# Performance work log

Hardware: AMD Instinct MI355X
Metric: run time of the kernel (lower is better)

## Reference

```python
import jax, jax.numpy as jnp
import numpy as np

B, C, L, H, W_SP = 4, 768, 8, 14, 14
HEADS = 12
HD = C // HEADS  # 64
SCALE = HD ** (-0.5)


def setup_inputs() -> dict:
    key = jax.random.key(0)
    ks = jax.random.split(key, 8)
    return {
        "q": jax.random.normal(ks[0], (B, C, L, H, W_SP), dtype=jnp.float32),
        "k": jax.random.normal(ks[1], (B, C, L, H, W_SP), dtype=jnp.float32),
        "v": jax.random.normal(ks[2], (B, C, L, H, W_SP), dtype=jnp.float32),
        "cls_q": jax.random.normal(ks[3], (B, C), dtype=jnp.float32),
        "cls_k": jax.random.normal(ks[4], (B, C), dtype=jnp.float32),
        "cls_v": jax.random.normal(ks[5], (B, C), dtype=jnp.float32),
        "W": jax.random.normal(ks[6], (C, C), dtype=jnp.float32) * 0.02,
        "b": jnp.zeros((C,), dtype=jnp.float32),
    }


def _split_heads(t):
    # 'b (head c) l h w -> b head (l h w) c'
    Bx = t.shape[0]
    return t.reshape(Bx, HEADS, HD, -1).transpose(0, 1, 3, 2)


def _split_cls(t):
    # 'b (head c) -> b head 1 c'
    return t.reshape(t.shape[0], HEADS, 1, HD)


def reference(q, k, v, cls_q, cls_k, cls_v, W, b):
    out_l, out_h, out_w = q.shape[2], q.shape[3], q.shape[4]
    qh = jnp.concatenate([_split_cls(cls_q), _split_heads(q)], axis=2)  # [B,head,S,c]
    kh = jnp.concatenate([_split_cls(cls_k), _split_heads(k)], axis=2)
    vh = jnp.concatenate([_split_cls(cls_v), _split_heads(v)], axis=2)
    attn = jnp.einsum('bhqc,bhkc->bhqk', qh, kh) * SCALE  # [B,head,S,S]
    attn = jax.nn.softmax(attn, axis=-1)
    x = jnp.einsum('bhqk,bhkc->bhqc', attn, vh)           # [B,head,S,c]
    Bx, _, S, _ = x.shape
    x = x.transpose(0, 2, 1, 3).reshape(Bx, S, HEADS * HD)  # 'b h s c -> b s (h c)'
    x = x @ W.T + b  # nn.Linear
    class_token = x[:, 0, :]
    x = x[:, 1:, :]
    # 'b (l h w) c -> b c l h w'
    x = x.transpose(0, 2, 1).reshape(Bx, HEADS * HD, out_l, out_h, out_w)
    return (x, class_token)
```

## Files before the change

### kernel.cpp

```cpp
#include <hip/hip_runtime.h>
#include <hip/hip_bf16.h>

#define NSP   1568
#define SEQ   1569
#define CDIM  768
#define NHEAD 12
#define NTOT  6276
#define BATCH 4
#define NBH   48
#define SPADQ 1664
#define SPADK 1664

typedef __bf16 bf16x8 __attribute__((ext_vector_type(8)));
typedef float  f32x4  __attribute__((ext_vector_type(4)));

static __device__ __forceinline__ unsigned pkbf(float a, float b) {
    __hip_bfloat16 ha = __float2bfloat16(a), hb = __float2bfloat16(b);
    return (unsigned)*(unsigned short*)&ha | ((unsigned)*(unsigned short*)&hb << 16);
}

__global__ __launch_bounds__(256) void pack_all(
    const float* __restrict__ qg, const float* __restrict__ kg,
    const float* __restrict__ vg, const float* __restrict__ cq,
    const float* __restrict__ ck, const float* __restrict__ cv,
    const float* __restrict__ W,
    __hip_bfloat16* __restrict__ Qb, __hip_bfloat16* __restrict__ Kb,
    __hip_bfloat16* __restrict__ Vb, __hip_bfloat16* __restrict__ Wb)
{
    const int t  = threadIdx.x;
    const int z  = blockIdx.z;

    if (z == 3) {
        const int id = blockIdx.y * 26 + blockIdx.x;
        if (id >= 288) return;
        const size_t i = ((size_t)id * 256 + t) * 8;
        const float4 a = *(const float4*)(W + i);
        const float4 c = *(const float4*)(W + i + 4);
        __hip_bfloat16 hh[8] = {
            __float2bfloat16(a.x), __float2bfloat16(a.y),
            __float2bfloat16(a.z), __float2bfloat16(a.w),
            __float2bfloat16(c.x), __float2bfloat16(c.y),
            __float2bfloat16(c.z), __float2bfloat16(c.w)};
        *(uint4*)(Wb + i) = *(const uint4*)hh;
        return;
    }

    const int st = blockIdx.x;
    const int bh = blockIdx.y;
    const int b = bh / NHEAD, h = bh % NHEAD;

    if (z == 2) {
        const float* g = vg + ((size_t)b * CDIM + h * 64) * NSP;
        const float* c = cv + b * CDIM + h * 64;
        const int sl = t & 63, s = st * 64 + sl;
        for (int i = 0; i < 16; ++i) {
            const int d = (t >> 6) * 16 + i;
            float v = 0.f;
            if (s == 0)       v = c[d];
            else if (s < SEQ) v = g[(size_t)d * NSP + s - 1];
            Vb[((size_t)bh * 64 + d) * SPADK + s] = __float2bfloat16(v);
        }
        return;
    }

    __shared__ float tile[64 * 65];
    const float* g = (z ? kg : qg) + ((size_t)b * CDIM + h * 64) * NSP;
    const float* c = (z ? ck : cq) + b * CDIM + h * 64;
    const float scale = z ? 1.f : 0.125f * 1.44269504f;

    const int sl = t & 63, s = st * 64 + sl;
    for (int i = 0; i < 16; ++i) {
        const int d = (t >> 6) * 16 + i;
        float v = 0.f;
        if (s == 0)       v = c[d];
        else if (s < SEQ) v = g[(size_t)d * NSP + s - 1];
        tile[d * 65 + sl] = v * scale;
    }
    __syncthreads();
    __hip_bfloat16* out = z ? Kb : Qb;
    const size_t rowbase = (size_t)bh * (z ? SPADK : SPADQ) + st * 64;
    const int d = t & 63;
    for (int i = 0; i < 16; ++i) {
        const int r = i * 4 + (t >> 6);
        out[(rowbase + r) * 64 + d] = __float2bfloat16(tile[d * 65 + r]);
    }
}

__global__ __launch_bounds__(256, 3) void attn_mfma(
    const __hip_bfloat16* __restrict__ Qbp, const __hip_bfloat16* __restrict__ Kbp,
    const __hip_bfloat16* __restrict__ Vbp, __hip_bfloat16* __restrict__ xb)
{
    __shared__ char smem[49152];
    char* const Ksb0 = smem;
    char* const Ksb1 = smem + 16384;

    const int t    = threadIdx.x;
    const int lane = t & 63;
    const int w    = t >> 6;
    const int lo   = lane & 15, hi = lane >> 4;

    const int gid  = blockIdx.x;
    const int slot = gid >> 3;
    const int bh   = (gid & 7) + 8 * (slot / 13);
    const int qb   = (slot % 13) * 128;
    const int b    = bh / NHEAD, h = bh % NHEAD;

    const unsigned short* Qg = (const unsigned short*)Qbp + ((size_t)bh * SPADQ + qb) * 64;
    const unsigned short* Kg = (const unsigned short*)Kbp + (size_t)bh * SPADK * 64;
    const unsigned short* Vg = (const unsigned short*)Vbp + (size_t)bh * 64 * SPADK;

    char* const Pw = smem + 32768 + w * 4096;

    bf16x8 qf[2][2];
    #pragma unroll
    for (int qn = 0; qn < 2; ++qn)
        #pragma unroll
        for (int ks = 0; ks < 2; ++ks)
            qf[qn][ks] = *(const bf16x8*)(Qg + (w * 32 + qn * 16 + lo) * 64 + (ks * 4 + hi) * 8);

    f32x4 o[2][4];
    f32x4 l5[2];
    #pragma unroll
    for (int m = 0; m < 2; ++m) {
        l5[m] = (f32x4){0.f, 0.f, 0.f, 0.f};
        #pragma unroll
        for (int n = 0; n < 4; ++n) o[m][n] = (f32x4){0.f, 0.f, 0.f, 0.f};
    }

    bf16x8 ones;
    #pragma unroll
    for (int i = 0; i < 8; ++i) ones[i] = (__bf16)1.0f;

    const int sr = t >> 3, sc = t & 7;

    uint4 kreg[4];
    #pragma unroll
    for (int p = 0; p < 4; ++p)
        kreg[p] = *(const uint4*)(Kg + (size_t)(sr + 32 * p) * 64 + sc * 8);
    #pragma unroll
    for (int p = 0; p < 4; ++p) {
        const int r = sr + 32 * p;
        *(uint4*)(Ksb0 + r * 128 + ((sc ^ (r & 7)) * 16)) = kreg[p];
    }

    int cur = 0;

    for (int it = 0; it < 13; ++it) {
        __syncthreads();
        char* const Kcur = cur ? Ksb1 : Ksb0;
        char* const Knxt = cur ? Ksb0 : Ksb1;

        const int itn = (it + 1 < 13) ? it + 1 : it;
        #pragma unroll
        for (int p = 0; p < 4; ++p)
            kreg[p] = *(const uint4*)(Kg + (size_t)(itn * 128 + sr + 32 * p) * 64 + sc * 8);

        #pragma unroll
        for (int sub = 0; sub < 2; ++sub) {
            const int kb = it * 128 + sub * 64;
            char* const Ksub = Kcur + sub * 8192;

            uint4 vf0[4];
            #pragma unroll
            for (int dn = 0; dn < 4; ++dn)
                vf0[dn] = *(const uint4*)(Vg + (size_t)(dn * 16 + lo) * SPADK + kb + hi * 8);

            f32x4 s[4][2];
            #pragma unroll
            for (int km = 0; km < 4; ++km)
                #pragma unroll
                for (int qn = 0; qn < 2; ++qn) s[km][qn] = (f32x4){0.f, 0.f, 0.f, 0.f};
            __builtin_amdgcn_s_setprio(1);
            #pragma unroll
            for (int ks = 0; ks < 2; ++ks) {
                bf16x8 ak[4];
                #pragma unroll
                for (int km = 0; km < 4; ++km)
                    ak[km] = *(const bf16x8*)(Ksub + (km * 16 + lo) * 128 + (((ks * 4 + hi) ^ (lo & 7)) * 16));
                #pragma unroll
                for (int km = 0; km < 4; ++km)
                    #pragma unroll
                    for (int qn = 0; qn < 2; ++qn)
                        s[km][qn] = __builtin_amdgcn_mfma_f32_16x16x32_bf16(ak[km], qf[qn][ks], s[km][qn], 0, 0, 0);
            }
            __builtin_amdgcn_s_setprio(0);

            if (it == 12) {
                #pragma unroll
                for (int km = 0; km < 4; ++km)
                    #pragma unroll
                    for (int r = 0; r < 4; ++r)
                        if (kb + km * 16 + hi * 4 + r >= SEQ) {
                            s[km][0][r] = -1e30f;
                            s[km][1][r] = -1e30f;
                        }
            }

            #pragma unroll
            for (int qn = 0; qn < 2; ++qn)
                #pragma unroll
                for (int km = 0; km < 4; ++km) {
                    const float p0 = exp2f(s[km][qn][0]);
                    const float p1 = exp2f(s[km][qn][1]);
                    const float p2 = exp2f(s[km][qn][2]);
                    const float p3 = exp2f(s[km][qn][3]);
                    uint2 pk;
                    pk.x = pkbf(p0, p1);
                    pk.y = pkbf(p2, p3);
                    const int row = qn * 16 + lo;
                    *(uint2*)(Pw + row * 128 + (((km * 2 + (hi >> 1)) ^ (lo & 7)) * 16) + (hi & 1) * 8) = pk;
                }

            uint4 vf1[4];
            #pragma unroll
            for (int dn = 0; dn < 4; ++dn)
                vf1[dn] = *(const uint4*)(Vg + (size_t)(dn * 16 + lo) * SPADK + kb + 32 + hi * 8);

            __builtin_amdgcn_s_setprio(1);
            #pragma unroll
            for (int ks = 0; ks < 2; ++ks) {
                bf16x8 ap[2];
                #pragma unroll
                for (int m = 0; m < 2; ++m)
                    ap[m] = *(const bf16x8*)(Pw + (m * 16 + lo) * 128 + (((ks * 4 + hi) ^ (lo & 7)) * 16));
                #pragma unroll
                for (int m = 0; m < 2; ++m) {
                    #pragma unroll
                    for (int dn = 0; dn < 4; ++dn) {
                        const bf16x8 bv = *(const bf16x8*)(ks ? &vf1[dn] : &vf0[dn]);
                        o[m][dn] = __builtin_amdgcn_mfma_f32_16x16x32_bf16(ap[m], bv, o[m][dn], 0, 0, 0);
                    }
                    l5[m] = __builtin_amdgcn_mfma_f32_16x16x32_bf16(ap[m], ones, l5[m], 0, 0, 0);
                }
            }
            __builtin_amdgcn_s_setprio(0);
        }

        #pragma unroll
        for (int p = 0; p < 4; ++p) {
            const int r = sr + 32 * p;
            *(uint4*)(Knxt + r * 128 + ((sc ^ (r & 7)) * 16)) = kreg[p];
        }
        cur ^= 1;
    }

    #pragma unroll
    for (int m = 0; m < 2; ++m)
        #pragma unroll
        for (int r = 0; r < 4; ++r) {
            const float inv = 1.f / l5[m][r];
            const int q = qb + w * 32 + m * 16 + hi * 4 + r;
            if (q < SEQ) {
                __hip_bfloat16* dst = xb + ((size_t)b * SEQ + q) * CDIM + h * 64 + lo;
                #pragma unroll
                for (int dn = 0; dn < 4; ++dn)
                    dst[dn * 16] = __float2bfloat16(o[m][dn][r] * inv);
            }
        }
}

__global__ __launch_bounds__(256) void proj_mfma(
    const __hip_bfloat16* __restrict__ Wb, const __hip_bfloat16* __restrict__ xbp,
    const float* __restrict__ bias, float* __restrict__ xout,
    float* __restrict__ clsout)
{
    __shared__ char smem[24576];
    char* Ws = smem;
    char* Xs = smem + 16384;

    const int t    = threadIdx.x;
    const int lane = t & 63;
    const int w    = t >> 6;
    const int lo   = lane & 15, hi = lane >> 4;
    const int nb   = blockIdx.x * 64;
    const int mb   = blockIdx.y * 128;

    const unsigned short* Wg = (const unsigned short*)Wb  + (size_t)mb * CDIM;
    const unsigned short* Xg = (const unsigned short*)xbp + (size_t)nb * CDIM;

    f32x4 acc[4][2];
    #pragma unroll
    for (int m = 0; m < 4; ++m)
        #pragma unroll
        for (int n = 0; n < 2; ++n) acc[m][n] = (f32x4){0.f, 0.f, 0.f, 0.f};

    const bool xok[2] = { nb + ((t)       >> 3) < NTOT,
                          nb + ((t + 256) >> 3) < NTOT };
    uint4 wreg[4], xreg[2];
    #pragma unroll
    for (int p = 0; p < 4; ++p) {
        const int ch = t + 256 * p;
        wreg[p] = *(const uint4*)(Wg + (ch >> 3) * CDIM + (ch & 7) * 8);
    }
    #pragma unroll
    for (int p = 0; p < 2; ++p) {
        const int ch = t + 256 * p;
        xreg[p] = xok[p] ? *(const uint4*)(Xg + (ch >> 3) * CDIM + (ch & 7) * 8)
                         : (uint4){0u, 0u, 0u, 0u};
    }

    for (int kt = 0; kt < 12; ++kt) {
        __syncthreads();
        #pragma unroll
        for (int p = 0; p < 4; ++p) {
            const int ch = t + 256 * p;
            const int r = ch >> 3, c = ch & 7;
            *(uint4*)(Ws + r * 128 + ((c ^ (r & 7)) * 16)) = wreg[p];
        }
        #pragma unroll
        for (int p = 0; p < 2; ++p) {
            const int ch = t + 256 * p;
            const int r = ch >> 3, c = ch & 7;
            *(uint4*)(Xs + r * 128 + ((c ^ (r & 7)) * 16)) = xreg[p];
        }
        __syncthreads();
        if (kt + 1 < 12) {
            const int kb = (kt + 1) * 64;
            #pragma unroll
            for (int p = 0; p < 4; ++p) {
                const int ch = t + 256 * p;
                wreg[p] = *(const uint4*)(Wg + (ch >> 3) * CDIM + kb + (ch & 7) * 8);
            }
            #pragma unroll
            for (int p = 0; p < 2; ++p) {
                const int ch = t + 256 * p;
                xreg[p] = xok[p] ? *(const uint4*)(Xg + (ch >> 3) * CDIM + kb + (ch & 7) * 8)
                                 : (uint4){0u, 0u, 0u, 0u};
            }
        }
        #pragma unroll
        for (int ks = 0; ks < 2; ++ks) {
            bf16x8 aw[4], bx[2];
            #pragma unroll
            for (int m = 0; m < 4; ++m) {
                const int row = (w >> 1) * 64 + m * 16 + lo;
                aw[m] = *(const bf16x8*)(Ws + row * 128 + (((ks * 4 + hi) ^ (lo & 7)) * 16));
            }
            #pragma unroll
            for (int n = 0; n < 2; ++n) {
                const int row = (w & 1) * 32 + n * 16 + lo;
                bx[n] = *(const bf16x8*)(Xs + row * 128 + (((ks * 4 + hi) ^ (lo & 7)) * 16));
            }
            #pragma unroll
            for (int m = 0; m < 4; ++m)
                #pragma unroll
                for (int n = 0; n < 2; ++n)
                    acc[m][n] = __builtin_amdgcn_mfma_f32_16x16x32_bf16(aw[m], bx[n], acc[m][n], 0, 0, 0);
        }
    }

    const int cob = mb + (w >> 1) * 64;
    const int nbb = nb + (w & 1) * 32;
    #pragma unroll
    for (int m = 0; m < 4; ++m)
        #pragma unroll
        for (int r = 0; r < 4; ++r) {
            const int co = cob + m * 16 + hi * 4 + r;
            const float bv = bias[co];
            #pragma unroll
            for (int n4 = 0; n4 < 2; ++n4) {
                const int n = nbb + n4 * 16 + lo;
                if (n >= NTOT) continue;
                const int bq = n / SEQ;
                const int s  = n - bq * SEQ;
                const float val = acc[m][n4][r] + bv;
                if (s == 0) clsout[bq * CDIM + co] = val;
                else        xout[((size_t)bq * CDIM + co) * NSP + (s - 1)] = val;
            }
        }
}

extern "C" void kernel_launch(void* const* d_in, const int* in_sizes, int n_in,
                              void* d_out, int out_size, void* d_ws, size_t ws_size,
                              hipStream_t stream)
{
    const float* q  = (const float*)d_in[0];
    const float* k  = (const float*)d_in[1];
    const float* v  = (const float*)d_in[2];
    const float* cq = (const float*)d_in[3];
    const float* ck = (const float*)d_in[4];
    const float* cv = (const float*)d_in[5];
    const float* W  = (const float*)d_in[6];
    const float* bi = (const float*)d_in[7];

    float* out    = (float*)d_out;
    float* xout   = out;
    float* clsout = out + (size_t)BATCH * CDIM * NSP;

    __hip_bfloat16* Qb = (__hip_bfloat16*)d_ws;
    __hip_bfloat16* Kb = Qb + (size_t)NBH * SPADQ * 64;
    __hip_bfloat16* Vb = Kb + (size_t)NBH * SPADK * 64;
    __hip_bfloat16* Wb = Vb + (size_t)NBH * 64 * SPADK;
    __hip_bfloat16* xb = Wb + (size_t)CDIM * CDIM;

    pack_all <<<dim3(26, NBH, 4), 256, 0, stream>>>(q, k, v, cq, ck, cv, W,
                                                    Qb, Kb, Vb, Wb);
    attn_mfma<<<dim3(624),        256, 0, stream>>>(Qb, Kb, Vb, xb);
    proj_mfma<<<dim3(99, 6),      256, 0, stream>>>(Wb, xb, bi, xout, clsout);
}
```

Measured before the change: 152.8 us.

## Fuse Q packing into attention kernel and remap projection block order

Result: no change. 152.6 us (-0.1%).

```diff
diff --git a/kernel.cpp b/kernel.cpp
--- a/kernel.cpp
+++ b/kernel.cpp
@@ -20,17 +20,16 @@
 }
 
 __global__ __launch_bounds__(256) void pack_all(
-    const float* __restrict__ qg, const float* __restrict__ kg,
-    const float* __restrict__ vg, const float* __restrict__ cq,
+    const float* __restrict__ kg, const float* __restrict__ vg,
     const float* __restrict__ ck, const float* __restrict__ cv,
     const float* __restrict__ W,
-    __hip_bfloat16* __restrict__ Qb, __hip_bfloat16* __restrict__ Kb,
-    __hip_bfloat16* __restrict__ Vb, __hip_bfloat16* __restrict__ Wb)
+    __hip_bfloat16* __restrict__ Kb, __hip_bfloat16* __restrict__ Vb,
+    __hip_bfloat16* __restrict__ Wb)
 {
     const int t  = threadIdx.x;
     const int z  = blockIdx.z;
 
-    if (z == 3) {
+    if (z == 2) {
         const int id = blockIdx.y * 26 + blockIdx.x;
         if (id >= 288) return;
         const size_t i = ((size_t)id * 256 + t) * 8;
@@ -49,7 +48,7 @@
     const int bh = blockIdx.y;
     const int b = bh / NHEAD, h = bh % NHEAD;
 
-    if (z == 2) {
+    if (z == 1) {
         const float* g = vg + ((size_t)b * CDIM + h * 64) * NSP;
         const float* c = cv + b * CDIM + h * 64;
         const int sl = t & 63, s = st * 64 + sl;
@@ -64,9 +63,8 @@
     }
 
     __shared__ float tile[64 * 65];
-    const float* g = (z ? kg : qg) + ((size_t)b * CDIM + h * 64) * NSP;
-    const float* c = (z ? ck : cq) + b * CDIM + h * 64;
-    const float scale = z ? 1.f : 0.125f * 1.44269504f;
+    const float* g = kg + ((size_t)b * CDIM + h * 64) * NSP;
+    const float* c = ck + b * CDIM + h * 64;
 
     const int sl = t & 63, s = st * 64 + sl;
     for (int i = 0; i < 16; ++i) {
@@ -74,21 +72,21 @@
         float v = 0.f;
         if (s == 0)       v = c[d];
         else if (s < SEQ) v = g[(size_t)d * NSP + s - 1];
-        tile[d * 65 + sl] = v * scale;
+        tile[d * 65 + sl] = v;
     }
     __syncthreads();
-    __hip_bfloat16* out = z ? Kb : Qb;
-    const size_t rowbase = (size_t)bh * (z ? SPADK : SPADQ) + st * 64;
+    const size_t rowbase = (size_t)bh * SPADK + st * 64;
     const int d = t & 63;
     for (int i = 0; i < 16; ++i) {
         const int r = i * 4 + (t >> 6);
-        out[(rowbase + r) * 64 + d] = __float2bfloat16(tile[d * 65 + r]);
+        Kb[(rowbase + r) * 64 + d] = __float2bfloat16(tile[d * 65 + r]);
     }
 }
 
 __global__ __launch_bounds__(256, 3) void attn_mfma(
-    const __hip_bfloat16* __restrict__ Qbp, const __hip_bfloat16* __restrict__ Kbp,
-    const __hip_bfloat16* __restrict__ Vbp, __hip_bfloat16* __restrict__ xb)
+    const float* __restrict__ qg, const float* __restrict__ cq,
+    const __hip_bfloat16* __restrict__ Kbp, const __hip_bfloat16* __restrict__ Vbp,
+    __hip_bfloat16* __restrict__ xb)
 {
     __shared__ char smem[49152];
     char* const Ksb0 = smem;
@@ -105,31 +103,10 @@
     const int qb   = (slot % 13) * 128;
     const int b    = bh / NHEAD, h = bh % NHEAD;
 
-    const unsigned short* Qg = (const unsigned short*)Qbp + ((size_t)bh * SPADQ + qb) * 64;
     const unsigned short* Kg = (const unsigned short*)Kbp + (size_t)bh * SPADK * 64;
     const unsigned short* Vg = (const unsigned short*)Vbp + (size_t)bh * 64 * SPADK;
 
     char* const Pw = smem + 32768 + w * 4096;
-
-    bf16x8 qf[2][2];
-    #pragma unroll
-    for (int qn = 0; qn < 2; ++qn)
-        #pragma unroll
-        for (int ks = 0; ks < 2; ++ks)
-            qf[qn][ks] = *(const bf16x8*)(Qg + (w * 32 + qn * 16 + lo) * 64 + (ks * 4 + hi) * 8);
-
-    f32x4 o[2][4];
-    f32x4 l5[2];
-    #pragma unroll
-    for (int m = 0; m < 2; ++m) {
-        l5[m] = (f32x4){0.f, 0.f, 0.f, 0.f};
-        #pragma unroll
-        for (int n = 0; n < 4; ++n) o[m][n] = (f32x4){0.f, 0.f, 0.f, 0.f};
-    }
-
-    bf16x8 ones;
-    #pragma unroll
-    for (int i = 0; i < 8; ++i) ones[i] = (__bf16)1.0f;
 
     const int sr = t >> 3, sc = t & 7;
 
@@ -142,6 +119,39 @@
         const int r = sr + 32 * p;
         *(uint4*)(Ksb0 + r * 128 + ((sc ^ (r & 7)) * 16)) = kreg[p];
     }
+
+    const float* qc = qg + ((size_t)b * CDIM + h * 64) * NSP;
+    const float* cc = cq + b * CDIM + h * 64;
+    const float qscale = 0.125f * 1.44269504f;
+    bf16x8 qf[2][2];
+    #pragma unroll
+    for (int qn = 0; qn < 2; ++qn) {
+        const int qglob = qb + w * 32 + qn * 16 + lo;
+        #pragma unroll
+        for (int ks = 0; ks < 2; ++ks)
+            #pragma unroll
+            for (int i = 0; i < 8; ++i) {
+                const int d = (ks * 4 + hi) * 8 + i;
+                float v = 0.f;
+                if (qglob == 0)       v = cc[d];
+                else if (qglob < SEQ) v = qc[(size_t)d * NSP + qglob - 1];
+                __hip_bfloat16 hv = __float2bfloat16(v * qscale);
+                qf[qn][ks][i] = *(__bf16*)&hv;
+            }
+    }
+
+    f32x4 o[2][4];
+    f32x4 l5[2];
+    #pragma unroll
+    for (int m = 0; m < 2; ++m) {
+        l5[m] = (f32x4){0.f, 0.f, 0.f, 0.f};
+        #pragma unroll
+        for (int n = 0; n < 4; ++n) o[m][n] = (f32x4){0.f, 0.f, 0.f, 0.f};
+    }
+
+    bf16x8 ones;
+    #pragma unroll
+    for (int i = 0; i < 8; ++i) ones[i] = (__bf16)1.0f;
 
     int cur = 0;
 
@@ -268,12 +278,15 @@
     char* Ws = smem;
     char* Xs = smem + 16384;
 
+    const int id = ((int)blockIdx.x & 7) * 75 + ((int)blockIdx.x >> 3);
+    if (id >= 594) return;
+    const int mb = (id / 99) * 128;
+    const int nb = (id % 99) * 64;
+
     const int t    = threadIdx.x;
     const int lane = t & 63;
     const int w    = t >> 6;
     const int lo   = lane & 15, hi = lane >> 4;
-    const int nb   = blockIdx.x * 64;
-    const int mb   = blockIdx.y * 128;
 
     const unsigned short* Wg = (const unsigned short*)Wb  + (size_t)mb * CDIM;
     const unsigned short* Xg = (const unsigned short*)xbp + (size_t)nb * CDIM;
@@ -387,14 +400,12 @@
     float* xout   = out;
     float* clsout = out + (size_t)BATCH * CDIM * NSP;
 
-    __hip_bfloat16* Qb = (__hip_bfloat16*)d_ws;
-    __hip_bfloat16* Kb = Qb + (size_t)NBH * SPADQ * 64;
+    __hip_bfloat16* Kb = (__hip_bfloat16*)d_ws;
     __hip_bfloat16* Vb = Kb + (size_t)NBH * SPADK * 64;
     __hip_bfloat16* Wb = Vb + (size_t)NBH * 64 * SPADK;
     __hip_bfloat16* xb = Wb + (size_t)CDIM * CDIM;
 
-    pack_all <<<dim3(26, NBH, 4), 256, 0, stream>>>(q, k, v, cq, ck, cv, W,
-                                                    Qb, Kb, Vb, Wb);
-    attn_mfma<<<dim3(624),        256, 0, stream>>>(Qb, Kb, Vb, xb);
-    proj_mfma<<<dim3(99, 6),      256, 0, stream>>>(Wb, xb, bi, xout, clsout);
+    pack_all <<<dim3(26, NBH, 3), 256, 0, stream>>>(k, v, ck, cv, W, Kb, Vb, Wb);
+    attn_mfma<<<dim3(624),        256, 0, stream>>>(q, cq, Kb, Vb, xb);
+    proj_mfma<<<dim3(600),        256, 0, stream>>>(Wb, xb, bi, xout, clsout);
 }
```

## Move cls token to sequence end for aligned vectorized packing; remap proj grid

Applied to the files above, without the earlier changes.

Measured after the change: 151.0 us. About the same (-1.2%).

```diff
diff --git a/kernel.cpp b/kernel.cpp
--- a/kernel.cpp
+++ b/kernel.cpp
@@ -52,37 +52,69 @@
     if (z == 2) {
         const float* g = vg + ((size_t)b * CDIM + h * 64) * NSP;
         const float* c = cv + b * CDIM + h * 64;
+        if (st < 24) {
+            const int s0 = st * 64 + (t & 15) * 4;
+            const int dr = t >> 4;
+            #pragma unroll
+            for (int i = 0; i < 4; ++i) {
+                const int d = dr + i * 16;
+                const float4 v4 = *(const float4*)(g + (size_t)d * NSP + s0);
+                __hip_bfloat16 hv[4] = {
+                    __float2bfloat16(v4.x), __float2bfloat16(v4.y),
+                    __float2bfloat16(v4.z), __float2bfloat16(v4.w)};
+                *(uint2*)(Vb + ((size_t)bh * 64 + d) * SPADK + s0) = *(const uint2*)hv;
+            }
+        } else {
+            const int s = st * 64 + (t & 63);
+            for (int i = 0; i < 16; ++i) {
+                const int d = (t >> 6) * 16 + i;
+                float v = 0.f;
+                if (s < NSP)       v = g[(size_t)d * NSP + s];
+                else if (s == NSP) v = c[d];
+                Vb[((size_t)bh * 64 + d) * SPADK + s] = __float2bfloat16(v);
+            }
+        }
+        return;
+    }
+
+    __shared__ float tile[64 * 68];
+    const float* g = (z ? kg : qg) + ((size_t)b * CDIM + h * 64) * NSP;
+    const float* c = (z ? ck : cq) + b * CDIM + h * 64;
+    const float scale = z ? 1.f : 0.125f * 1.44269504f;
+
+    if (st < 24) {
+        const int sq = (t & 15) * 4;
+        const int s0 = st * 64 + sq;
+        const int dr = t >> 4;
+        #pragma unroll
+        for (int i = 0; i < 4; ++i) {
+            const int d = dr + i * 16;
+            float4 v4 = *(const float4*)(g + (size_t)d * NSP + s0);
+            v4.x *= scale; v4.y *= scale; v4.z *= scale; v4.w *= scale;
+            *(float4*)(&tile[d * 68 + sq]) = v4;
+        }
+    } else {
         const int sl = t & 63, s = st * 64 + sl;
         for (int i = 0; i < 16; ++i) {
             const int d = (t >> 6) * 16 + i;
             float v = 0.f;
-            if (s == 0)       v = c[d];
-            else if (s < SEQ) v = g[(size_t)d * NSP + s - 1];
-            Vb[((size_t)bh * 64 + d) * SPADK + s] = __float2bfloat16(v);
-        }
-        return;
-    }
-
-    __shared__ float tile[64 * 65];
-    const float* g = (z ? kg : qg) + ((size_t)b * CDIM + h * 64) * NSP;
-    const float* c = (z ? ck : cq) + b * CDIM + h * 64;
-    const float scale = z ? 1.f : 0.125f * 1.44269504f;
-
-    const int sl = t & 63, s = st * 64 + sl;
-    for (int i = 0; i < 16; ++i) {
-        const int d = (t >> 6) * 16 + i;
-        float v = 0.f;
-        if (s == 0)       v = c[d];
-        else if (s < SEQ) v = g[(size_t)d * NSP + s - 1];
-        tile[d * 65 + sl] = v * scale;
+            if (s < NSP)       v = g[(size_t)d * NSP + s];
+            else if (s == NSP) v = c[d];
+            tile[d * 68 + sl] = v * scale;
+        }
     }
     __syncthreads();
     __hip_bfloat16* out = z ? Kb : Qb;
     const size_t rowbase = (size_t)bh * (z ? SPADK : SPADQ) + st * 64;
-    const int d = t & 63;
-    for (int i = 0; i < 16; ++i) {
-        const int r = i * 4 + (t >> 6);
-        out[(rowbase + r) * 64 + d] = __float2bfloat16(tile[d * 65 + r]);
+    const int dg = (t & 7) * 8;
+    #pragma unroll
+    for (int half = 0; half < 2; ++half) {
+        const int r = (t >> 3) + half * 32;
+        __hip_bfloat16 hv[8];
+        #pragma unroll
+        for (int j = 0; j < 8; ++j)
+            hv[j] = __float2bfloat16(tile[(dg + j) * 68 + r]);
+        *(uint4*)(out + (rowbase + r) * 64 + dg) = *(const uint4*)hv;
     }
 }
 
@@ -249,9 +281,10 @@
         #pragma unroll
         for (int r = 0; r < 4; ++r) {
             const float inv = 1.f / l5[m][r];
-            const int q = qb + w * 32 + m * 16 + hi * 4 + r;
-            if (q < SEQ) {
-                __hip_bfloat16* dst = xb + ((size_t)b * SEQ + q) * CDIM + h * 64 + lo;
+            const int qp = qb + w * 32 + m * 16 + hi * 4 + r;
+            if (qp < SEQ) {
+                const int sq = (qp == NSP) ? 0 : qp + 1;
+                __hip_bfloat16* dst = xb + ((size_t)b * SEQ + sq) * CDIM + h * 64 + lo;
                 #pragma unroll
                 for (int dn = 0; dn < 4; ++dn)
                     dst[dn * 16] = __float2bfloat16(o[m][dn][r] * inv);
@@ -268,12 +301,15 @@
     char* Ws = smem;
     char* Xs = smem + 16384;
 
+    const int id = ((int)blockIdx.x & 7) * 75 + ((int)blockIdx.x >> 3);
+    if (id >= 594) return;
+    const int mb = (id / 99) * 128;
+    const int nb = (id % 99) * 64;
+
     const int t    = threadIdx.x;
     const int lane = t & 63;
     const int w    = t >> 6;
     const int lo   = lane & 15, hi = lane >> 4;
-    const int nb   = blockIdx.x * 64;
-    const int mb   = blockIdx.y * 128;
 
     const unsigned short* Wg = (const unsigned short*)Wb  + (size_t)mb * CDIM;
     const unsigned short* Xg = (const unsigned short*)xbp + (size_t)nb * CDIM;
@@ -396,5 +432,5 @@
     pack_all <<<dim3(26, NBH, 4), 256, 0, stream>>>(q, k, v, cq, ck, cv, W,
                                                     Qb, Kb, Vb, Wb);
     attn_mfma<<<dim3(624),        256, 0, stream>>>(Qb, Kb, Vb, xb);
-    proj_mfma<<<dim3(99, 6),      256, 0, stream>>>(Wb, xb, bi, xout, clsout);
+    proj_mfma<<<dim3(600),        256, 0, stream>>>(Wb, xb, bi, xout, clsout);
 }
```
